# Performance work log

Hardware: AMD Instinct MI355X
Metric: run time of the kernel (lower is better)

## Reference

```python
import jax, jax.numpy as jnp
import numpy as np

SCENE = (128, 128, 8)      # (X, Y, Z) voxel grid
VOXEL_SIZE = 0.4
DOWNSAMPLE_Z = 2
NUM_HEADS = 8
NUM_POINTS = 4
LN_EPS = 1e-5


def _pix2vox(depth, K, E, voxel_origin):
    # depth [1,H,W]; K [1,3,3]; E [1,4,4]; voxel_origin [1,3]
    B, H, W = depth.shape
    gx, gy = jnp.meshgrid(jnp.arange(W, dtype=depth.dtype), jnp.arange(H, dtype=depth.dtype))
    pix = jnp.stack([gx, gy])                              # [2,H,W] -> (u, v) after flip in torch
    d = depth[:, None]                                     # [B,1,H,W]
    p_x = jnp.concatenate([pix[None] * d, d], 1).reshape(B, 3, -1)
    p_c = jnp.linalg.inv(K) @ p_x                          # camera coords [B,3,HW]
    p_c = jnp.concatenate([p_c, jnp.ones_like(p_c[:, :1])], 1)
    p_w = jnp.linalg.inv(E) @ p_c                          # world coords [B,4,HW]
    p_v = (jnp.swapaxes(p_w[:, :3], 1, 2) - voxel_origin[:, None, :]) / VOXEL_SIZE - 0.5
    p_v = p_v.at[..., 2].set(p_v[..., 2] / DOWNSAMPLE_Z)
    return jnp.trunc(p_v).astype(jnp.int32)               # torch .long() truncates toward 0


def _voxel_mask(p_v):
    X, Y, Z = SCENE
    p = p_v[0]                                             # [HW,3] (batch asserted == 1)
    valid = ((p[:, 0] >= 0) & (p[:, 0] < X) & (p[:, 1] >= 0) & (p[:, 1] < Y)
             & (p[:, 2] >= 0) & (p[:, 2] < Z))
    flat = jnp.where(valid, (p[:, 0] * Y + p[:, 1]) * Z + p[:, 2], 0)
    return jnp.zeros(X * Y * Z, dtype=bool).at[flat].max(valid)


def _ms_deform_attn(q, feats, ref, Wv, bv, Woff, boff, Wattw, battw, Wout, bout):
    # q [N,C]; feats: list of [C,Hl,Wl]; ref [N,2] normalized (shared across levels)
    N, C = q.shape
    hd = C // NUM_HEADS
    shapes = [(f.shape[1], f.shape[2]) for f in feats]
    L = len(feats)
    flat = jnp.concatenate([f.reshape(C, -1).T for f in feats], 0)      # [Lsum, C]
    value = (flat @ Wv.T + bv).reshape(-1, NUM_HEADS, hd)               # [Lsum, h, hd]
    off = (q @ Woff.T + boff).reshape(N, NUM_HEADS, L, NUM_POINTS, 2)
    w = jax.nn.softmax((q @ Wattw.T + battw).reshape(N, NUM_HEADS, L * NUM_POINTS), -1)
    w = w.reshape(N, NUM_HEADS, L, NUM_POINTS)
    normalizer = jnp.array([[wl, hl] for (hl, wl) in shapes], dtype=q.dtype)  # (W,H) per level
    loc = ref[:, None, None, None, :] + off / normalizer[None, None, :, None, :]
    h_idx = jnp.arange(NUM_HEADS)[None, :, None]
    out = jnp.zeros((N, NUM_HEADS, hd), q.dtype)
    start = 0
    for lvl, (Hl, Wl) in enumerate(shapes):
        v = value[start:start + Hl * Wl]                   # [Hl*Wl, h, hd]
        start += Hl * Wl
        # grid_sample bilinear, align_corners=False, zero padding
        x = loc[:, :, lvl, :, 0] * Wl - 0.5                # [N,h,P]
        y = loc[:, :, lvl, :, 1] * Hl - 0.5
        x0 = jnp.floor(x); y0 = jnp.floor(y)
        lx = x - x0; ly = y - y0
        x0i = x0.astype(jnp.int32); y0i = y0.astype(jnp.int32)
        samp = jnp.zeros((N, NUM_HEADS, NUM_POINTS, hd), q.dtype)
        for dy, dx, wgt in ((0, 0, (1 - lx) * (1 - ly)), (0, 1, lx * (1 - ly)),
                            (1, 0, (1 - lx) * ly), (1, 1, lx * ly)):
            xi = x0i + dx; yi = y0i + dy
            ok = (xi >= 0) & (xi < Wl) & (yi >= 0) & (yi < Hl)
            idx = jnp.where(ok, yi * Wl + xi, 0)
            g = v[idx, h_idx]                              # [N,h,P,hd] per-head gather
            samp = samp + g * (wgt * ok)[..., None]
        out = out + jnp.einsum('nhp,nhpd->nhd', w[:, :, lvl], samp)
    return out.reshape(N, C) @ Wout.T + bout


def _forward(scene_embed, feat0, feat1, feat2, depth, K, E, voxel_origin, ref_pix,
             Wv, bv, Woff, boff, Wattw, battw, Wout, bout, ln_g, ln_b):
    X, Y, Z = SCENE
    mask = _voxel_mask(_pix2vox(depth, K, E, voxel_origin))             # [N] bool
    q = scene_embed[0]                                                  # [N,C]
    attn = _ms_deform_attn(q, [feat0[0], feat1[0], feat2[0]], ref_pix[0],
                           Wv, bv, Woff, boff, Wattw, battw, Wout, bout)
    h = q + attn                                                        # residual (MSDeformAttn identity)
    mu = jnp.mean(h, -1, keepdims=True)
    var = jnp.mean((h - mu) ** 2, -1, keepdims=True)
    h = (h - mu) / jnp.sqrt(var + LN_EPS) * ln_g + ln_b                 # post-norm
    out = jnp.where(mask[:, None], h, q)                                # index_fov_back_to_voxels
    return out.T.reshape(1, -1, X, Y, Z)                                # nlc -> nchw [1,C,X,Y,Z]


def setup_inputs() -> dict:
    key = jax.random.key(0)
    ks = jax.random.split(key, 12)
    X, Y, Z = SCENE
    N = X * Y * Z
    C = 128
    H, W = 192, 640
    s = 0.02
    scene_embed = jax.random.normal(ks[0], (1, N, C), jnp.float32)
    feat0 = jax.random.normal(ks[1], (1, C, 48, 160), jnp.float32)
    feat1 = jax.random.normal(ks[2], (1, C, 24, 80), jnp.float32)
    feat2 = jax.random.normal(ks[3], (1, C, 12, 40), jnp.float32)
    depth = jax.random.uniform(ks[4], (1, H, W), jnp.float32, 1.0, 40.0)
    K = jnp.array([[[552.55, 0.0, 320.0], [0.0, 552.55, 96.0], [0.0, 0.0, 1.0]]], jnp.float32)
    E = jnp.eye(4, dtype=jnp.float32)[None]
    voxel_origin = jnp.array([[-25.6, -3.2, 0.0]], jnp.float32)
    ref_pix = jax.random.uniform(ks[5], (1, N, 2), jnp.float32)
    return {
        'scene_embed': scene_embed, 'feat0': feat0, 'feat1': feat1, 'feat2': feat2,
        'depth': depth, 'K': K, 'E': E, 'voxel_origin': voxel_origin, 'ref_pix': ref_pix,
        'Wv': jax.random.normal(ks[6], (C, C), jnp.float32) * s,
        'bv': jnp.zeros((C,), jnp.float32),
        'Woff': jax.random.normal(ks[7], (NUM_HEADS * 3 * NUM_POINTS * 2, C), jnp.float32) * s,
        'boff': jnp.zeros((NUM_HEADS * 3 * NUM_POINTS * 2,), jnp.float32),
        'Wattw': jax.random.normal(ks[8], (NUM_HEADS * 3 * NUM_POINTS, C), jnp.float32) * s,
        'battw': jnp.zeros((NUM_HEADS * 3 * NUM_POINTS,), jnp.float32),
        'Wout': jax.random.normal(ks[9], (C, C), jnp.float32) * s,
        'bout': jnp.zeros((C,), jnp.float32),
        'ln_g': jnp.ones((C,), jnp.float32),
        'ln_b': jnp.zeros((C,), jnp.float32),
    }


def reference(scene_embed, feat0, feat1, feat2, depth, K, E, voxel_origin, ref_pix,
              Wv, bv, Woff, boff, Wattw, battw, Wout, bout, ln_g, ln_b):
    return _forward(scene_embed, feat0, feat1, feat2, depth, K, E, voxel_origin, ref_pix,
                    Wv, bv, Woff, boff, Wattw, battw, Wout, bout, ln_g, ln_b)
```

## Files before the change

### kernel.cpp

```cpp
#include <hip/hip_runtime.h>
#include <hip/hip_bf16.h>
#include <stdint.h>

#define XS 128
#define YS 128
#define ZS 8
#define NQ (XS*YS*ZS)
#define CDIM 128
#define NH 8
#define HD 16
#define DH 192
#define DW 640
#define NPIX (DH*DW)
#define NVPIX 10080

typedef float f32x4 __attribute__((ext_vector_type(4)));
typedef short s16x8 __attribute__((ext_vector_type(8)));

__device__ __forceinline__ float b2f(unsigned short u){
    union { unsigned int i; float f; } v; v.i = ((unsigned int)u) << 16; return v.f;
}
__device__ __forceinline__ unsigned short f2b(float f){
    __hip_bfloat16 h = __float2bfloat16(f);
    return *reinterpret_cast<unsigned short*>(&h);
}
__device__ __forceinline__ float blo(unsigned int u){
    union { unsigned int i; float f; } v; v.i = u << 16; return v.f;
}
__device__ __forceinline__ float bhi(unsigned int u){
    union { unsigned int i; float f; } v; v.i = u & 0xffff0000u; return v.f;
}

__global__ __launch_bounds__(256)
void inv_kernel(const float* __restrict__ K,
                const float* __restrict__ E,
                double* __restrict__ inv_out,
                const float* __restrict__ Woff,
                const float* __restrict__ Wattw,
                const float* __restrict__ Wout,
                unsigned short* __restrict__ Wbf){
    if (blockIdx.x != 0){
        int idx = (blockIdx.x-1)*256 + threadIdx.x;
        if (idx < 24576)      Wbf[idx] = f2b(Woff[idx]);
        else if (idx < 36864) Wbf[idx] = f2b(Wattw[idx-24576]);
        else if (idx < 53248) Wbf[idx] = f2b(Wout[idx-36864]);
        return;
    }
    if (threadIdx.x != 0) return;
    double k[3][3], e[4][4];
    for (int i=0;i<9;i++)  k[i/3][i%3] = (double)K[i];
    for (int i=0;i<16;i++) e[i/4][i%4] = (double)E[i];
    double det = k[0][0]*(k[1][1]*k[2][2]-k[1][2]*k[2][1])
               - k[0][1]*(k[1][0]*k[2][2]-k[1][2]*k[2][0])
               + k[0][2]*(k[1][0]*k[2][1]-k[1][1]*k[2][0]);
    double id = 1.0/det;
    double inv[3][3];
    inv[0][0]=(k[1][1]*k[2][2]-k[1][2]*k[2][1])*id;
    inv[0][1]=(k[0][2]*k[2][1]-k[0][1]*k[2][2])*id;
    inv[0][2]=(k[0][1]*k[1][2]-k[0][2]*k[1][1])*id;
    inv[1][0]=(k[1][2]*k[2][0]-k[1][0]*k[2][2])*id;
    inv[1][1]=(k[0][0]*k[2][2]-k[0][2]*k[2][0])*id;
    inv[1][2]=(k[0][2]*k[1][0]-k[0][0]*k[1][2])*id;
    inv[2][0]=(k[1][0]*k[2][1]-k[1][1]*k[2][0])*id;
    inv[2][1]=(k[0][1]*k[2][0]-k[0][0]*k[2][1])*id;
    inv[2][2]=(k[0][0]*k[1][1]-k[0][1]*k[1][0])*id;
    for (int i=0;i<9;i++) inv_out[i] = inv[i/3][i%3];
    double a[4][8];
    for (int i=0;i<4;i++){ for(int j=0;j<4;j++){ a[i][j]=e[i][j]; a[i][4+j]=(i==j)?1.0:0.0; } }
    for (int c=0;c<4;c++){
        int piv=c; double best=fabs(a[c][c]);
        for (int r=c+1;r<4;r++){ double v=fabs(a[r][c]); if (v>best){best=v;piv=r;} }
        if (piv!=c){ for (int j=0;j<8;j++){ double tmp=a[c][j]; a[c][j]=a[piv][j]; a[piv][j]=tmp; } }
        double pv = 1.0/a[c][c];
        for (int j=0;j<8;j++) a[c][j]*=pv;
        for (int r=0;r<4;r++){
            if (r==c) continue;
            double f=a[r][c];
            for(int j=0;j<8;j++) a[r][j]-=f*a[c][j];
        }
    }
    for (int i=0;i<16;i++) inv_out[9+i] = a[i/4][4 + (i%4)];
}

__global__ __launch_bounds__(256)
void prep_kernel(const float* __restrict__ q_in,
                 const unsigned short* __restrict__ Wbf,
                 const float* __restrict__ boff,
                 const float* __restrict__ battw,
                 unsigned short* __restrict__ offawB,
                 int nOff, int nVal,
                 const float* __restrict__ f0,
                 const float* __restrict__ f1,
                 const float* __restrict__ f2,
                 const float* __restrict__ Wv,
                 const float* __restrict__ bv,
                 unsigned short* __restrict__ value,
                 const float* __restrict__ depth,
                 const double* __restrict__ invm,
                 const float* __restrict__ vorigin,
                 unsigned char* __restrict__ mask){
    __shared__ __align__(16) unsigned char smem[36864 + 1280];
    const int t = threadIdx.x;

    if ((int)blockIdx.x < nOff){
        unsigned short* Ob   = (unsigned short*)smem;
        float*          bias = (float*)(smem + 36864);
        const int n0 = blockIdx.x * 64;
        for (int idx = t; idx < 288; idx += 256)
            bias[idx] = (idx < 192) ? boff[idx] : battw[idx-192];

        const int w = t >> 6, lane = t & 63, lr = lane & 15, lg = lane >> 4;
        const int qq = w*16 + lr;

        f32x4 acc[18];
        #pragma unroll
        for (int i=0;i<18;i++) acc[i] = (f32x4){0.f,0.f,0.f,0.f};

        const float* qrow = q_in + (size_t)(n0 + qq)*CDIM;
        #pragma unroll
        for (int ks=0; ks<4; ++ks){
            const float* qp = qrow + ks*32 + lg*8;
            float4 qa = *(const float4*)(qp);
            float4 qb = *(const float4*)(qp+4);
            union { s16x8 v; unsigned short s[8]; } bf;
            bf.s[0]=f2b(qa.x); bf.s[1]=f2b(qa.y); bf.s[2]=f2b(qa.z); bf.s[3]=f2b(qa.w);
            bf.s[4]=f2b(qb.x); bf.s[5]=f2b(qb.y); bf.s[6]=f2b(qb.z); bf.s[7]=f2b(qb.w);
            const unsigned short* wp = Wbf + (size_t)lr*CDIM + ks*32 + lg*8;
            #pragma unroll
            for (int nt=0; nt<18; ++nt){
                s16x8 af = *(const s16x8*)(wp + nt*16*CDIM);
                acc[nt] = __builtin_amdgcn_mfma_f32_16x16x32_bf16(af, bf.v, acc[nt], 0, 0, 0);
            }
        }
        __syncthreads();

        #pragma unroll
        for (int nt=0; nt<18; ++nt){
            #pragma unroll
            for (int r=0; r<4; ++r){
                int f = nt*16 + lg*4 + r;
                float v = acc[nt][r] + bias[f];
                Ob[(qq>>3)*2304 + f*8 + (qq&7)] = f2b(v);
            }
        }
        __syncthreads();

        for (int task = t; task < 512; task += 256){
            int q = task >> 3, h = task & 7;
            unsigned short* p = Ob + (q>>3)*2304 + (192 + h*12)*8 + (q&7);
            float e[12]; float m = -1e30f;
            #pragma unroll
            for (int i=0;i<12;i++){ e[i] = b2f(p[i*8]); m = fmaxf(m, e[i]); }
            float s = 0.f;
            #pragma unroll
            for (int i=0;i<12;i++){ e[i] = __expf(e[i]-m); s += e[i]; }
            float is = 1.f/s;
            #pragma unroll
            for (int i=0;i<12;i++) p[i*8] = f2b(e[i]*is);
        }
        __syncthreads();

        {
            const uint4* src = (const uint4*)Ob;
            uint4* dst = (uint4*)(offawB + (size_t)blockIdx.x * 18432);
            for (int idx = t; idx < 2304; idx += 256) dst[idx] = src[idx];
        }
    } else if ((int)blockIdx.x < nOff + nVal){
        const int half = t >> 7, tt = t & 127;
        const int p0 = (blockIdx.x - nOff)*8 + half*4;
        float (*fl)[4] = (float(*)[4])((float*)smem + half*(CDIM*4));
        const float* src; int hw, lp;
        if (p0 < 7680)      { src=f0; hw=7680; lp=p0; }
        else if (p0 < 9600) { src=f1; hw=1920; lp=p0-7680; }
        else                { src=f2; hw=480;  lp=p0-9600; }
        float4 v = *(const float4*)(src + tt*hw + lp);
        fl[tt][0]=v.x; fl[tt][1]=v.y; fl[tt][2]=v.z; fl[tt][3]=v.w;
        __syncthreads();
        float bb = bv[tt];
        float acc[4] = {bb,bb,bb,bb};
        const float4* wrow = (const float4*)(Wv + tt*CDIM);
        #pragma unroll 8
        for (int kc=0; kc<32; ++kc){
            float4 w = wrow[kc];
            #pragma unroll
            for (int u=0;u<4;u++){
                float wu = (u==0)?w.x:(u==1)?w.y:(u==2)?w.z:w.w;
                float4 fv = *(const float4*)fl[kc*4+u];
                acc[0] += fv.x*wu; acc[1] += fv.y*wu; acc[2] += fv.z*wu; acc[3] += fv.w*wu;
            }
        }
        const int hh = tt >> 4, cc = tt & 15;
        #pragma unroll
        for (int i=0;i<4;i++)
            value[((size_t)hh*NVPIX + (size_t)(p0+i))*HD + cc] = f2b(acc[i]);
    } else {
        int tid = (blockIdx.x - nOff - nVal)*256 + t;
        if (tid >= NPIX) return;
        int gx = tid % DW, gy = tid / DW;
        double d  = (double)depth[tid];
        double X0 = (double)gx * d, X1 = (double)gy * d, X2 = d;
        double c0 = invm[0]*X0 + invm[1]*X1 + invm[2]*X2;
        double c1 = invm[3]*X0 + invm[4]*X1 + invm[5]*X2;
        double c2 = invm[6]*X0 + invm[7]*X1 + invm[8]*X2;
        const double* iE = invm + 9;
        double w0 = iE[0]*c0 + iE[1]*c1 + iE[2]*c2  + iE[3];
        double w1 = iE[4]*c0 + iE[5]*c1 + iE[6]*c2  + iE[7];
        double w2 = iE[8]*c0 + iE[9]*c1 + iE[10]*c2 + iE[11];
        double v0 = (w0-(double)vorigin[0])/0.4 - 0.5;
        double v1 = (w1-(double)vorigin[1])/0.4 - 0.5;
        double v2 = ((w2-(double)vorigin[2])/0.4 - 0.5) / 2.0;
        int xi = (int)v0, yi = (int)v1, zi = (int)v2;
        if (xi>=0 && xi<XS && yi>=0 && yi<YS && zi>=0 && zi<ZS)
            mask[(xi*YS + yi)*ZS + zi] = 1;
    }
}

__global__ __launch_bounds__(256, 2)
void attn_kernel(const float* __restrict__ q_in,
                 const float* __restrict__ refpix,
                 const unsigned short* __restrict__ offawB,
                 const unsigned short* __restrict__ value,
                 const unsigned short* __restrict__ WoutBf,
                 const float* __restrict__ bout,
                 const float* __restrict__ lng,
                 const float* __restrict__ lnb,
                 const unsigned char* __restrict__ mask,
                 float* __restrict__ dout,
                 int q0g){
    const int n0l = blockIdx.x * 8;
    const int n0g = q0g + n0l;
    const int t = threadIdx.x;
    __shared__ __align__(16) unsigned char smem[25296];
    unsigned short* raw   = (unsigned short*)(smem);
    unsigned char*  descB = smem + 4608;
    float*          out2  = (float*)(smem + 4608);
    unsigned char*  obfB  = smem + 16896;
    float (*q_s)[CDIM]    = (float(*)[CDIM])(smem + 20992);
    float*          rp_s  = (float*)(smem + 25088);
    float*          wredp = (float*)(smem + 25152);
    unsigned char*  mask_s= (unsigned char*)(smem + 25280);

    {
        const unsigned int* src = (const unsigned int*)(offawB + (size_t)(n0l>>3)*2304);
        unsigned int* dst = (unsigned int*)raw;
        #pragma unroll
        for (int i=0;i<5;i++){ int idx = t + i*256; if (idx < 1152) dst[idx] = src[idx]; }
        ((float4*)q_s)[t] = ((const float4*)(q_in + (size_t)n0g*CDIM))[t];
        ((unsigned int*)obfB)[512 + t] = 0;
        ((unsigned int*)obfB)[768 + t] = 0;
        if (t < 16) rp_s[t] = refpix[n0g*2 + t];
        if (t < 8)  mask_s[t] = mask[n0g + t];
    }
    __syncthreads();

    for (int idx = t; idx < 768; idx += 256){
        int q = idx & 7, hp = idx >> 3;
        int lp = hp % 12;
        float fw, fh; int Wl, Hl, st;
        if (lp < 4)      { fw=160.f; fh=48.f; Wl=160; Hl=48; st=0; }
        else if (lp < 8) { fw=80.f;  fh=24.f; Wl=80;  Hl=24; st=7680; }
        else             { fw=40.f;  fh=12.f; Wl=40;  Hl=12; st=9600; }
        float offx = b2f(raw[(hp*2)*8 + q]);
        float offy = b2f(raw[(hp*2+1)*8 + q]);
        float aw   = b2f(raw[(192+hp)*8 + q]);
        float x = rp_s[q*2+0]*fw - 0.5f + offx;
        float y = rp_s[q*2+1]*fh - 0.5f + offy;
        float x0f = floorf(x), y0f = floorf(y);
        float lx = x-x0f, ly = y-y0f;
        int x0 = (int)x0f, y0 = (int)y0f;
        bool x0ok = (x0>=0)&&(x0<Wl), x1ok=(x0+1>=0)&&(x0+1<Wl);
        bool y0ok = (y0>=0)&&(y0<Hl), y1ok=(y0+1>=0)&&(y0+1<Hl);
        float w00 = (x0ok&&y0ok)? (1.f-lx)*(1.f-ly)*aw : 0.f;
        float w01 = (x1ok&&y0ok)? lx*(1.f-ly)*aw       : 0.f;
        float w10 = (x0ok&&y1ok)? (1.f-lx)*ly*aw       : 0.f;
        float w11 = (x1ok&&y1ok)? lx*ly*aw             : 0.f;
        int yc0 = min(max(y0,0),Hl-1), yc1 = min(max(y0+1,0),Hl-1);
        int xc0 = min(max(x0,0),Wl-1), xc1 = min(max(x0+1,0),Wl-1);
        unsigned int rb0 = (unsigned int)(st + yc0*Wl), rb1 = (unsigned int)(st + yc1*Wl);
        uint4 d;
        d.x = (rb0+(unsigned int)xc0) | ((rb0+(unsigned int)xc1)<<16);
        d.y = (rb1+(unsigned int)xc0) | ((rb1+(unsigned int)xc1)<<16);
        d.z = (unsigned int)f2b(w00) | ((unsigned int)f2b(w01)<<16);
        d.w = (unsigned int)f2b(w10) | ((unsigned int)f2b(w11)<<16);
        *(uint4*)(descB + (((unsigned int)(idx ^ ((idx>>5)&7)))<<4)) = d;
    }
    __syncthreads();

    {
        const int cp = t & 7, hs = (t>>3) & 7, qgs = t >> 6;
        const unsigned short* vh = value + ((size_t)hs*NVPIX)*HD + cp*2;
        float av0x=0.f, av0y=0.f, av1x=0.f, av1y=0.f;
        #pragma unroll
        for (int lp=0; lp<12; ++lp){
            #pragma unroll
            for (int qi2=0; qi2<2; ++qi2){
                int idx = (hs*12+lp)*8 + qgs*2 + qi2;
                uint4 d = *(const uint4*)(descB + (((unsigned int)(idx ^ ((idx>>5)&7)))<<4));
                unsigned int p00 = d.x & 0xffffu, p01 = d.x >> 16;
                unsigned int p10 = d.y & 0xffffu, p11 = d.y >> 16;
                unsigned int u00 = *(const unsigned int*)(vh + (p00<<4));
                unsigned int u01 = *(const unsigned int*)(vh + (p01<<4));
                unsigned int u10 = *(const unsigned int*)(vh + (p10<<4));
                unsigned int u11 = *(const unsigned int*)(vh + (p11<<4));
                float w00 = blo(d.z), w01 = bhi(d.z), w10 = blo(d.w), w11 = bhi(d.w);
                float sx = blo(u00)*w00 + blo(u01)*w01 + blo(u10)*w10 + blo(u11)*w11;
                float sy = bhi(u00)*w00 + bhi(u01)*w01 + bhi(u10)*w10 + bhi(u11)*w11;
                if (qi2 == 0){ av0x += sx; av0y += sy; }
                else         { av1x += sx; av1y += sy; }
            }
        }
        const int q0q = qgs*2;
        unsigned int pk0 = (unsigned int)f2b(av0x) | ((unsigned int)f2b(av0y)<<16);
        unsigned int pk1 = (unsigned int)f2b(av1x) | ((unsigned int)f2b(av1y)<<16);
        unsigned int bo0 = (unsigned int)(q0q*256 + hs*32 + cp*4)     ^ (unsigned int)((q0q&7)<<4);
        unsigned int bo1 = (unsigned int)((q0q+1)*256 + hs*32 + cp*4) ^ (unsigned int)(((q0q+1)&7)<<4);
        *(unsigned int*)(obfB + bo0) = pk0;
        *(unsigned int*)(obfB + bo1) = pk1;
    }
    __syncthreads();

    {
        const int w = t >> 6, lane = t & 63, lr = lane & 15, lg = lane >> 4;
        f32x4 a0 = (f32x4){0.f,0.f,0.f,0.f};
        f32x4 a1 = (f32x4){0.f,0.f,0.f,0.f};
        #pragma unroll
        for (int ks=0; ks<4; ++ks){
            unsigned int bo = (unsigned int)(lr*256 + ks*64 + lg*16) ^ (unsigned int)((lr&7)<<4);
            s16x8 bfrag = *(const s16x8*)(obfB + bo);
            const unsigned short* wp = WoutBf + (size_t)(w*32 + lr)*CDIM + ks*32 + lg*8;
            s16x8 af0 = *(const s16x8*)(wp);
            s16x8 af1 = *(const s16x8*)(wp + 16*CDIM);
            a0 = __builtin_amdgcn_mfma_f32_16x16x32_bf16(af0, bfrag, a0, 0, 0, 0);
            a1 = __builtin_amdgcn_mfma_f32_16x16x32_bf16(af1, bfrag, a1, 0, 0, 0);
        }
        if (lr < 8){
            int f0 = w*32 + lg*4;
            float4 b0 = *(const float4*)(bout + f0);
            float4 b1 = *(const float4*)(bout + f0 + 16);
            float4 v0, v1;
            v0.x = a0[0]+b0.x; v0.y = a0[1]+b0.y; v0.z = a0[2]+b0.z; v0.w = a0[3]+b0.w;
            v1.x = a1[0]+b1.x; v1.y = a1[1]+b1.y; v1.z = a1[2]+b1.z; v1.w = a1[3]+b1.w;
            *(float4*)(out2 + lr*CDIM + f0)      = v0;
            *(float4*)(out2 + lr*CDIM + f0 + 16) = v1;
        }
    }
    __syncthreads();

    const int r = t & 127;
    const int qb = t >> 7;
    const int wv = t >> 6;
    float acc[4];
    #pragma unroll
    for (int qi4=0;qi4<4;qi4++) acc[qi4] = out2[(qb*4+qi4)*CDIM + r];

    float hv[4], sred[4];
    #pragma unroll
    for (int qi4=0;qi4<4;qi4++){ hv[qi4] = q_s[qb*4+qi4][r] + acc[qi4]; sred[qi4]=hv[qi4]; }
    #pragma unroll
    for (int off=32; off>0; off>>=1)
        #pragma unroll
        for (int qi4=0;qi4<4;qi4++) sred[qi4] += __shfl_xor(sred[qi4], off, 64);
    if ((t&63)==0){
        #pragma unroll
        for (int qi4=0;qi4<4;qi4++) wredp[0*16 + wv*4 + qi4]=sred[qi4];
    }
    __syncthreads();
    float mu[4], dv[4];
    #pragma unroll
    for (int qi4=0;qi4<4;qi4++){
        mu[qi4] = (wredp[0*16 + (qb*2)*4 + qi4]+wredp[0*16 + (qb*2+1)*4 + qi4]) * (1.f/128.f);
        dv[qi4] = hv[qi4]-mu[qi4];
        sred[qi4] = dv[qi4]*dv[qi4];
    }
    #pragma unroll
    for (int off=32; off>0; off>>=1)
        #pragma unroll
        for (int qi4=0;qi4<4;qi4++) sred[qi4] += __shfl_xor(sred[qi4], off, 64);
    if ((t&63)==0){
        #pragma unroll
        for (int qi4=0;qi4<4;qi4++) wredp[1*16 + wv*4 + qi4]=sred[qi4];
    }
    __syncthreads();

    float res[4];
    const float g = lng[r], b = lnb[r];
    #pragma unroll
    for (int qi4=0;qi4<4;qi4++){
        float var = (wredp[1*16 + (qb*2)*4 + qi4]+wredp[1*16 + (qb*2+1)*4 + qi4]) * (1.f/128.f);
        float nv  = dv[qi4] * __frsqrt_rn(var + 1e-5f) * g + b;
        res[qi4] = mask_s[qb*4+qi4] ? nv : q_s[qb*4+qi4][r];
    }
    float4 o; o.x=res[0]; o.y=res[1]; o.z=res[2]; o.w=res[3];
    *(float4*)(dout + (size_t)r*NQ + n0g + qb*4) = o;
}

extern "C" void kernel_launch(void* const* d_in, const int* in_sizes, int n_in,
                              void* d_out, int out_size, void* d_ws, size_t ws_size,
                              hipStream_t stream){
    const float* scene  = (const float*)d_in[0];
    const float* f0     = (const float*)d_in[1];
    const float* f1     = (const float*)d_in[2];
    const float* f2     = (const float*)d_in[3];
    const float* depth  = (const float*)d_in[4];
    const float* K      = (const float*)d_in[5];
    const float* E      = (const float*)d_in[6];
    const float* vorig  = (const float*)d_in[7];
    const float* refpix = (const float*)d_in[8];
    const float* Wv     = (const float*)d_in[9];
    const float* bv     = (const float*)d_in[10];
    const float* Woff   = (const float*)d_in[11];
    const float* boff   = (const float*)d_in[12];
    const float* Wattw  = (const float*)d_in[13];
    const float* battw  = (const float*)d_in[14];
    const float* Wout   = (const float*)d_in[15];
    const float* bout   = (const float*)d_in[16];
    const float* lng    = (const float*)d_in[17];
    const float* lnb    = (const float*)d_in[18];

    char* ws = (char*)d_ws;
    const size_t FIXED = 512 + 131072 + 2580480 + 106496;
    double*         invm   = (double*)(ws);
    unsigned char*  mask   = (unsigned char*)(ws + 512);
    unsigned short* value  = (unsigned short*)(ws + 512 + 131072);
    unsigned short* Wbf    = (unsigned short*)(ws + 512 + 131072 + 2580480);
    unsigned short* WoutBf = Wbf + 36864;
    unsigned short* offawB = (unsigned short*)(ws + FIXED);

    size_t avail = (ws_size > FIXED) ? (ws_size - FIXED) : 0;
    long long maxq = (long long)(avail / (288*2));
    int chunk = (int)((maxq/64)*64);
    if (chunk > NQ) chunk = NQ;
    if (chunk < 64) chunk = 64;

    hipMemsetAsync(mask, 0, NQ, stream);
    inv_kernel<<<209, 256, 0, stream>>>(K, E, invm, Woff, Wattw, Wout, Wbf);

    for (int q0 = 0; q0 < NQ; q0 += chunk){
        int len = (NQ - q0 < chunk) ? (NQ - q0) : chunk;
        int nOff  = len/64;
        int nVal  = (q0 == 0) ? (NVPIX/8) : 0;
        int nMask = (q0 == 0) ? ((NPIX+255)/256) : 0;
        prep_kernel<<<nOff + nVal + nMask, 256, 0, stream>>>(
            scene + (size_t)q0*CDIM, Wbf, boff, battw, offawB,
            nOff, nVal,
            f0, f1, f2, Wv, bv, value,
            depth, invm, vorig, mask);
        attn_kernel<<<len/8, 256, 0, stream>>>(scene, refpix, offawB, value,
                                               WoutBf, bout, lng, lnb, mask,
                                               (float*)d_out, q0);
    }
}
```

Baseline: 468.2 us.

## Fuse offset/attention-weight projection and softmax into the attention kernel

Moves the query projection (offsets and attention logits via bf16 MFMA) and the per-head softmax from the prep kernel into the attention kernel, so each 8-query block computes its own 288 outputs in shared memory. This removes the global offawB intermediate buffer, its write and reread, and the chunked host loop. To fit 5 MFMA tiles per wave across 4 waves, the weight buffer is padded with a zero tile, which wastes some MFMA work on 8 unused query rows. The projection is now done at a granularity of 8 queries per block, which gives poorer MFMA utilisation.

```diff
diff --git a/kernel.cpp b/kernel.cpp
--- a/kernel.cpp
+++ b/kernel.cpp
@@ -43,7 +43,8 @@
         int idx = (blockIdx.x-1)*256 + threadIdx.x;
         if (idx < 24576)      Wbf[idx] = f2b(Woff[idx]);
         else if (idx < 36864) Wbf[idx] = f2b(Wattw[idx-24576]);
-        else if (idx < 53248) Wbf[idx] = f2b(Wout[idx-36864]);
+        else if (idx < 40960) Wbf[idx] = 0;
+        else if (idx < 57344) Wbf[idx] = f2b(Wout[idx-40960]);
         return;
     }
     if (threadIdx.x != 0) return;
@@ -83,92 +84,23 @@
 }
 
 __global__ __launch_bounds__(256)
-void prep_kernel(const float* __restrict__ q_in,
-                 const unsigned short* __restrict__ Wbf,
-                 const float* __restrict__ boff,
-                 const float* __restrict__ battw,
-                 unsigned short* __restrict__ offawB,
-                 int nOff, int nVal,
-                 const float* __restrict__ f0,
-                 const float* __restrict__ f1,
-                 const float* __restrict__ f2,
-                 const float* __restrict__ Wv,
-                 const float* __restrict__ bv,
-                 unsigned short* __restrict__ value,
-                 const float* __restrict__ depth,
-                 const double* __restrict__ invm,
-                 const float* __restrict__ vorigin,
-                 unsigned char* __restrict__ mask){
-    __shared__ __align__(16) unsigned char smem[36864 + 1280];
+void prep2_kernel(int nVal,
+                  const float* __restrict__ f0,
+                  const float* __restrict__ f1,
+                  const float* __restrict__ f2,
+                  const float* __restrict__ Wv,
+                  const float* __restrict__ bv,
+                  unsigned short* __restrict__ value,
+                  const float* __restrict__ depth,
+                  const double* __restrict__ invm,
+                  const float* __restrict__ vorigin,
+                  unsigned char* __restrict__ mask){
+    __shared__ float fl2[2][CDIM][4];
     const int t = threadIdx.x;
-
-    if ((int)blockIdx.x < nOff){
-        unsigned short* Ob   = (unsigned short*)smem;
-        float*          bias = (float*)(smem + 36864);
-        const int n0 = blockIdx.x * 64;
-        for (int idx = t; idx < 288; idx += 256)
-            bias[idx] = (idx < 192) ? boff[idx] : battw[idx-192];
-
-        const int w = t >> 6, lane = t & 63, lr = lane & 15, lg = lane >> 4;
-        const int qq = w*16 + lr;
-
-        f32x4 acc[18];
-        #pragma unroll
-        for (int i=0;i<18;i++) acc[i] = (f32x4){0.f,0.f,0.f,0.f};
-
-        const float* qrow = q_in + (size_t)(n0 + qq)*CDIM;
-        #pragma unroll
-        for (int ks=0; ks<4; ++ks){
-            const float* qp = qrow + ks*32 + lg*8;
-            float4 qa = *(const float4*)(qp);
-            float4 qb = *(const float4*)(qp+4);
-            union { s16x8 v; unsigned short s[8]; } bf;
-            bf.s[0]=f2b(qa.x); bf.s[1]=f2b(qa.y); bf.s[2]=f2b(qa.z); bf.s[3]=f2b(qa.w);
-            bf.s[4]=f2b(qb.x); bf.s[5]=f2b(qb.y); bf.s[6]=f2b(qb.z); bf.s[7]=f2b(qb.w);
-            const unsigned short* wp = Wbf + (size_t)lr*CDIM + ks*32 + lg*8;
-            #pragma unroll
-            for (int nt=0; nt<18; ++nt){
-                s16x8 af = *(const s16x8*)(wp + nt*16*CDIM);
-                acc[nt] = __builtin_amdgcn_mfma_f32_16x16x32_bf16(af, bf.v, acc[nt], 0, 0, 0);
-            }
-        }
-        __syncthreads();
-
-        #pragma unroll
-        for (int nt=0; nt<18; ++nt){
-            #pragma unroll
-            for (int r=0; r<4; ++r){
-                int f = nt*16 + lg*4 + r;
-                float v = acc[nt][r] + bias[f];
-                Ob[(qq>>3)*2304 + f*8 + (qq&7)] = f2b(v);
-            }
-        }
-        __syncthreads();
-
-        for (int task = t; task < 512; task += 256){
-            int q = task >> 3, h = task & 7;
-            unsigned short* p = Ob + (q>>3)*2304 + (192 + h*12)*8 + (q&7);
-            float e[12]; float m = -1e30f;
-            #pragma unroll
-            for (int i=0;i<12;i++){ e[i] = b2f(p[i*8]); m = fmaxf(m, e[i]); }
-            float s = 0.f;
-            #pragma unroll
-            for (int i=0;i<12;i++){ e[i] = __expf(e[i]-m); s += e[i]; }
-            float is = 1.f/s;
-            #pragma unroll
-            for (int i=0;i<12;i++) p[i*8] = f2b(e[i]*is);
-        }
-        __syncthreads();
-
-        {
-            const uint4* src = (const uint4*)Ob;
-            uint4* dst = (uint4*)(offawB + (size_t)blockIdx.x * 18432);
-            for (int idx = t; idx < 2304; idx += 256) dst[idx] = src[idx];
-        }
-    } else if ((int)blockIdx.x < nOff + nVal){
+    if ((int)blockIdx.x < nVal){
         const int half = t >> 7, tt = t & 127;
-        const int p0 = (blockIdx.x - nOff)*8 + half*4;
-        float (*fl)[4] = (float(*)[4])((float*)smem + half*(CDIM*4));
+        const int p0 = blockIdx.x*8 + half*4;
+        float (*fl)[4] = fl2[half];
         const float* src; int hw, lp;
         if (p0 < 7680)      { src=f0; hw=7680; lp=p0; }
         else if (p0 < 9600) { src=f1; hw=1920; lp=p0-7680; }
@@ -194,7 +126,7 @@
         for (int i=0;i<4;i++)
             value[((size_t)hh*NVPIX + (size_t)(p0+i))*HD + cc] = f2b(acc[i]);
     } else {
-        int tid = (blockIdx.x - nOff - nVal)*256 + t;
+        int tid = (blockIdx.x - nVal)*256 + t;
         if (tid >= NPIX) return;
         int gx = tid % DW, gy = tid / DW;
         double d  = (double)depth[tid];
@@ -216,22 +148,24 @@
 }
 
 __global__ __launch_bounds__(256, 2)
-void attn_kernel(const float* __restrict__ q_in,
-                 const float* __restrict__ refpix,
-                 const unsigned short* __restrict__ offawB,
-                 const unsigned short* __restrict__ value,
-                 const unsigned short* __restrict__ WoutBf,
-                 const float* __restrict__ bout,
-                 const float* __restrict__ lng,
-                 const float* __restrict__ lnb,
-                 const unsigned char* __restrict__ mask,
-                 float* __restrict__ dout,
-                 int q0g){
-    const int n0l = blockIdx.x * 8;
-    const int n0g = q0g + n0l;
+void attn_fused(const float* __restrict__ q_in,
+                const float* __restrict__ refpix,
+                const unsigned short* __restrict__ Wbf,
+                const float* __restrict__ boff,
+                const float* __restrict__ battw,
+                const unsigned short* __restrict__ value,
+                const unsigned short* __restrict__ WoutBf,
+                const float* __restrict__ bout,
+                const float* __restrict__ lng,
+                const float* __restrict__ lnb,
+                const unsigned char* __restrict__ mask,
+                float* __restrict__ dout){
+    const int n0g = blockIdx.x * 8;
     const int t = threadIdx.x;
     __shared__ __align__(16) unsigned char smem[25296];
-    unsigned short* raw   = (unsigned short*)(smem);
+    unsigned short* Ob    = (unsigned short*)(smem);
+    unsigned char*  qbfB  = smem + 4608;
+    float*          bias  = (float*)(smem + 6656);
     unsigned char*  descB = smem + 4608;
     float*          out2  = (float*)(smem + 4608);
     unsigned char*  obfB  = smem + 16896;
@@ -241,15 +175,67 @@
     unsigned char*  mask_s= (unsigned char*)(smem + 25280);
 
     {
-        const unsigned int* src = (const unsigned int*)(offawB + (size_t)(n0l>>3)*2304);
-        unsigned int* dst = (unsigned int*)raw;
-        #pragma unroll
-        for (int i=0;i<5;i++){ int idx = t + i*256; if (idx < 1152) dst[idx] = src[idx]; }
-        ((float4*)q_s)[t] = ((const float4*)(q_in + (size_t)n0g*CDIM))[t];
+        float4 qv = ((const float4*)(q_in + (size_t)n0g*CDIM))[t];
+        ((float4*)q_s)[t] = qv;
+        const int q = t >> 5;
+        unsigned int pk0 = (unsigned int)f2b(qv.x) | ((unsigned int)f2b(qv.y)<<16);
+        unsigned int pk1 = (unsigned int)f2b(qv.z) | ((unsigned int)f2b(qv.w)<<16);
+        unsigned int bo = (unsigned int)(q*256 + (t&31)*8) ^ (unsigned int)(q<<4);
+        *(unsigned int*)(qbfB + bo)     = pk0;
+        *(unsigned int*)(qbfB + bo + 4) = pk1;
+        for (int i=t;i<288;i+=256) bias[i] = (i<192)? boff[i] : battw[i-192];
         ((unsigned int*)obfB)[512 + t] = 0;
         ((unsigned int*)obfB)[768 + t] = 0;
         if (t < 16) rp_s[t] = refpix[n0g*2 + t];
         if (t < 8)  mask_s[t] = mask[n0g + t];
+    }
+    __syncthreads();
+
+    {
+        const int w = t >> 6, lane = t & 63, lr = lane & 15, lg = lane >> 4;
+        const int q = lr & 7;
+        const int nt0 = w*5;
+        f32x4 acc[5];
+        #pragma unroll
+        for (int i=0;i<5;i++) acc[i] = (f32x4){0.f,0.f,0.f,0.f};
+        #pragma unroll
+        for (int ks=0; ks<4; ++ks){
+            s16x8 bfrag = *(const s16x8*)(qbfB + (((unsigned int)(q*256 + ks*64 + lg*16)) ^ (unsigned int)(q<<4)));
+            const unsigned short* wp = Wbf + (size_t)(nt0*16 + lr)*CDIM + ks*32 + lg*8;
+            #pragma unroll
+            for (int j=0;j<5;++j){
+                s16x8 af = *(const s16x8*)(wp + j*16*CDIM);
+                acc[j] = __builtin_amdgcn_mfma_f32_16x16x32_bf16(af, bfrag, acc[j], 0, 0, 0);
+            }
+        }
+        if (lr < 8){
+            #pragma unroll
+            for (int j=0;j<5;++j){
+                int nt = nt0 + j;
+                if (nt < 18){
+                    #pragma unroll
+                    for (int r=0;r<4;++r){
+                        int f = nt*16 + lg*4 + r;
+                        Ob[f*8 + lr] = f2b(acc[j][r] + bias[f]);
+                    }
+                }
+            }
+        }
+    }
+    __syncthreads();
+
+    if (t < 64){
+        int q = t >> 3, h = t & 7;
+        unsigned short* p = Ob + (192 + h*12)*8 + q;
+        float e[12]; float m = -1e30f;
+        #pragma unroll
+        for (int i=0;i<12;i++){ e[i] = b2f(p[i*8]); m = fmaxf(m, e[i]); }
+        float s = 0.f;
+        #pragma unroll
+        for (int i=0;i<12;i++){ e[i] = __expf(e[i]-m); s += e[i]; }
+        float is = 1.f/s;
+        #pragma unroll
+        for (int i=0;i<12;i++) p[i*8] = f2b(e[i]*is);
     }
     __syncthreads();
 
@@ -260,9 +246,9 @@
         if (lp < 4)      { fw=160.f; fh=48.f; Wl=160; Hl=48; st=0; }
         else if (lp < 8) { fw=80.f;  fh=24.f; Wl=80;  Hl=24; st=7680; }
         else             { fw=40.f;  fh=12.f; Wl=40;  Hl=12; st=9600; }
-        float offx = b2f(raw[(hp*2)*8 + q]);
-        float offy = b2f(raw[(hp*2+1)*8 + q]);
-        float aw   = b2f(raw[(192+hp)*8 + q]);
+        float offx = b2f(Ob[(hp*2)*8 + q]);
+        float offy = b2f(Ob[(hp*2+1)*8 + q]);
+        float aw   = b2f(Ob[(192+hp)*8 + q]);
         float x = rp_s[q*2+0]*fw - 0.5f + offx;
         float y = rp_s[q*2+1]*fh - 0.5f + offy;
         float x0f = floorf(x), y0f = floorf(y);
@@ -418,35 +404,20 @@
     const float* lnb    = (const float*)d_in[18];
 
     char* ws = (char*)d_ws;
-    const size_t FIXED = 512 + 131072 + 2580480 + 106496;
     double*         invm   = (double*)(ws);
     unsigned char*  mask   = (unsigned char*)(ws + 512);
     unsigned short* value  = (unsigned short*)(ws + 512 + 131072);
     unsigned short* Wbf    = (unsigned short*)(ws + 512 + 131072 + 2580480);
-    unsigned short* WoutBf = Wbf + 36864;
-    unsigned short* offawB = (unsigned short*)(ws + FIXED);
-
-    size_t avail = (ws_size > FIXED) ? (ws_size - FIXED) : 0;
-    long long maxq = (long long)(avail / (288*2));
-    int chunk = (int)((maxq/64)*64);
-    if (chunk > NQ) chunk = NQ;
-    if (chunk < 64) chunk = 64;
+    unsigned short* WoutBf = Wbf + 40960;
 
     hipMemsetAsync(mask, 0, NQ, stream);
-    inv_kernel<<<209, 256, 0, stream>>>(K, E, invm, Woff, Wattw, Wout, Wbf);
-
-    for (int q0 = 0; q0 < NQ; q0 += chunk){
-        int len = (NQ - q0 < chunk) ? (NQ - q0) : chunk;
-        int nOff  = len/64;
-        int nVal  = (q0 == 0) ? (NVPIX/8) : 0;
-        int nMask = (q0 == 0) ? ((NPIX+255)/256) : 0;
-        prep_kernel<<<nOff + nVal + nMask, 256, 0, stream>>>(
-            scene + (size_t)q0*CDIM, Wbf, boff, battw, offawB,
-            nOff, nVal,
-            f0, f1, f2, Wv, bv, value,
-            depth, invm, vorig, mask);
-        attn_kernel<<<len/8, 256, 0, stream>>>(scene, refpix, offawB, value,
-                                               WoutBf, bout, lng, lnb, mask,
-                                               (float*)d_out, q0);
-    }
-}
+    inv_kernel<<<225, 256, 0, stream>>>(K, E, invm, Woff, Wattw, Wout, Wbf);
+
+    int nVal  = NVPIX/8;
+    int nMask = (NPIX+255)/256;
+    prep2_kernel<<<nVal + nMask, 256, 0, stream>>>(nVal, f0, f1, f2, Wv, bv, value,
+                                                   depth, invm, vorig, mask);
+    attn_fused<<<NQ/8, 256, 0, stream>>>(scene, refpix, Wbf, boff, battw, value,
+                                         WoutBf, bout, lng, lnb, mask,
+                                         (float*)d_out);
+}
```

Measured after the change: 491.5 us. +5.0%, slower.
